# Kernel optimization log

Hardware: AMD Instinct MI355X
Metric: run time of the kernel (lower is better)

The kernel has to match this reference:

```python
import jax, jax.numpy as jnp
import numpy as np
import math

B, N, DIM = 2, 4096, 256
NUM_HEADS = 8
HEAD_DIM = DIM // NUM_HEADS
WINDOW = 7  # default window_size in create_local_mask


def local_mask(seq_len: int, window_size: int = WINDOW) -> jnp.ndarray:
    """Boolean [N,N] mask: True where attention is allowed (2D grid locality)."""
    grid = int(math.isqrt(seq_len))
    idx = jnp.arange(seq_len)
    row, col = idx // grid, idx % grid
    half = window_size // 2
    ok_row = jnp.abs(row[:, None] - row[None, :]) <= half
    ok_col = jnp.abs(col[:, None] - col[None, :]) <= half
    return ok_row & ok_col


def setup_inputs() -> dict:
    key = jax.random.key(0)
    k1, k2, k3, k4 = jax.random.split(key, 4)
    x = jax.random.normal(k1, (B, N, DIM), dtype=jnp.float32)
    W_qkv = jax.random.normal(k2, (3 * DIM, DIM), dtype=jnp.float32) * (DIM ** -0.5)
    W_proj = jax.random.normal(k3, (DIM, DIM), dtype=jnp.float32) * (DIM ** -0.5)
    b_proj = jax.random.normal(k4, (DIM,), dtype=jnp.float32) * 0.01
    temperature = jnp.ones((1,), dtype=jnp.float32)
    return {"x": x, "W_qkv": W_qkv, "W_proj": W_proj, "b_proj": b_proj,
            "temperature": temperature}


def reference(x, W_qkv, W_proj, b_proj, temperature):
    Bb, Nn, C = x.shape
    scale = HEAD_DIM ** -0.5
    # qkv linear (no bias): [B,N,3C] -> [3,B,H,N,hd]
    qkv = (x @ W_qkv.T).reshape(Bb, Nn, 3, NUM_HEADS, HEAD_DIM)
    qkv = jnp.transpose(qkv, (2, 0, 3, 1, 4))
    q, k, v = qkv[0], qkv[1], qkv[2]
    # scores with learnable temperature
    attn = jnp.einsum('bhqd,bhkd->bhqk', q, k) * (scale * temperature[0])
    mask = local_mask(Nn)  # training path: N > 100 -> mask applied
    attn = jnp.where(mask[None, None, :, :], attn, -jnp.inf)
    attn = jax.nn.softmax(attn, axis=-1)
    out = jnp.einsum('bhqk,bhkd->bhqd', attn, v)  # [B,H,N,hd]
    out = jnp.transpose(out, (0, 2, 1, 3)).reshape(Bb, Nn, C)
    return out @ W_proj.T + b_proj
```

## Files before the change

kernel.cpp:

```cpp
#include <hip/hip_runtime.h>
#include <hip/hip_bf16.h>
#include <math.h>

#define DIM   256
#define NHEAD 8
#define HD    32
#define NTOK  4096
#define GRD   64
#define BATCH 2
#define MTOT  (BATCH * NTOK)
#define PLANE (NTOK * HD)

typedef __attribute__((ext_vector_type(8))) short bf16x8;
typedef __attribute__((ext_vector_type(4))) float f32x4;

static __device__ __forceinline__ unsigned short f2b(float f) {
  __hip_bfloat16 h = __float2bfloat16(f);
  union { __hip_bfloat16 h; unsigned short u; } cv;
  cv.h = h;
  return cv.u;
}

static __device__ __forceinline__ unsigned cvtpk_bf16(float lo, float hi) {
  unsigned r;
  asm("v_cvt_pk_bf16_f32 %0, %1, %2" : "=v"(r) : "v"(lo), "v"(hi));
  return r;
}

static __device__ __forceinline__ bf16x8 pack8(float4 a0, float4 a1) {
  union { bf16x8 v; unsigned short u[8]; } o;
  o.u[0] = f2b(a0.x); o.u[1] = f2b(a0.y); o.u[2] = f2b(a0.z); o.u[3] = f2b(a0.w);
  o.u[4] = f2b(a1.x); o.u[5] = f2b(a1.y); o.u[6] = f2b(a1.z); o.u[7] = f2b(a1.w);
  return o.v;
}

#define GLDS16(SRC, DST) __builtin_amdgcn_global_load_lds( \
    (const __attribute__((address_space(1))) void*)(SRC),  \
    (__attribute__((address_space(3))) void*)(DST), 16, 0, 0)

__global__ __launch_bounds__(256) void gemm_qkv(const float* __restrict__ A,
                                                const float* __restrict__ Bw,
                                                unsigned short* __restrict__ Cout) {
  const int K = 256;
  __shared__ __align__(16) char smem[34816];
  __hip_bfloat16* As = (__hip_bfloat16*)smem;
  __hip_bfloat16* Bs = (__hip_bfloat16*)(smem + 10240);
  const int tid = threadIdx.x;
  const int l = tid & 63, w = tid >> 6;
  const int bm = blockIdx.y * 128, bn = blockIdx.x * 128;
  const int wr = w >> 1, wc = w & 1;
  const int lr = l & 15, kh = l >> 4;
  const int lrow = l >> 2, lcol = (l & 3) * 8;

  f32x4 acc[4][4];
  #pragma unroll
  for (int i = 0; i < 4; ++i)
    #pragma unroll
    for (int j = 0; j < 4; ++j)
      acc[i][j] = (f32x4){0.f, 0.f, 0.f, 0.f};

  for (int k0 = 0; k0 < K; k0 += 32) {
    #pragma unroll
    for (int i = 0; i < 2; ++i) {
      const int r0 = (w * 2 + i) * 16;
      const float* ga = A  + (size_t)(bm + r0 + lrow) * K + k0 + lcol;
      const float* gb = Bw + (size_t)(bn + r0 + lrow) * K + k0 + lcol;
      float4 a0 = *(const float4*)ga, a1 = *(const float4*)(ga + 4);
      float4 b0 = *(const float4*)gb, b1 = *(const float4*)(gb + 4);
      *(bf16x8*)&As[(r0 + lrow) * 40 + lcol] = pack8(a0, a1);
      *(bf16x8*)&Bs[(r0 + lrow) * 40 + lcol] = pack8(b0, b1);
    }
    __syncthreads();

    bf16x8 af[4], bfr[4];
    #pragma unroll
    for (int f = 0; f < 4; ++f) {
      af[f]  = *(const bf16x8*)&As[(wr * 64 + f * 16 + lr) * 40 + kh * 8];
      bfr[f] = *(const bf16x8*)&Bs[(wc * 64 + f * 16 + lr) * 40 + kh * 8];
    }
    #pragma unroll
    for (int fi = 0; fi < 4; ++fi)
      #pragma unroll
      for (int fj = 0; fj < 4; ++fj)
        acc[fi][fj] = __builtin_amdgcn_mfma_f32_16x16x32_bf16(af[fi], bfr[fj], acc[fi][fj], 0, 0, 0);
    __syncthreads();
  }

  if (blockIdx.x < 4) {
    #pragma unroll
    for (int fi = 0; fi < 4; ++fi)
      #pragma unroll
      for (int fj = 0; fj < 4; ++fj)
        #pragma unroll
        for (int rr = 0; rr < 4; ++rr) {
          const int m = bm + wr * 64 + fi * 16 + kh * 4 + rr;
          const int n = bn + wc * 64 + fj * 16 + lr;
          const int sel = n >> 8, rem = n & 255;
          const int hh = rem >> 5, d = rem & 31;
          const int bb = m >> 12, tok = m & 4095;
          Cout[(size_t)(sel * 16 + bb * 8 + hh) * PLANE + tok * 32 + d] =
              f2b(acc[fi][fj][rr]);
        }
  } else {
    unsigned short* Ts = (unsigned short*)smem;
    #pragma unroll
    for (int fi = 0; fi < 4; ++fi)
      #pragma unroll
      for (int fj = 0; fj < 4; ++fj)
        #pragma unroll
        for (int rr = 0; rr < 4; ++rr) {
          const int tokl = wr * 64 + fi * 16 + kh * 4 + rr;
          const int dl   = wc * 64 + fj * 16 + lr;
          Ts[tokl * 136 + dl] = f2b(acc[fi][fj][rr]);
        }
    __syncthreads();
    const int dl = tid >> 1, th = (tid & 1) * 64;
    const int dg = (bn - 512) + dl;
    const int hh = dg >> 5, dd = dg & 31;
    const int bb = bm >> 12, tokb = bm & 4095;
    unsigned short* vt = Cout + (size_t)(32 + bb * 8 + hh) * PLANE + dd * 4096 + tokb + th;
    #pragma unroll
    for (int j = 0; j < 8; ++j) {
      union { bf16x8 v; unsigned short u[8]; } o;
      #pragma unroll
      for (int e = 0; e < 8; ++e)
        o.u[e] = Ts[(th + j * 8 + e) * 136 + dl];
      *(bf16x8*)(vt + j * 8) = o.v;
    }
  }
}

__global__ __launch_bounds__(256) void gemm_proj(const __hip_bfloat16* __restrict__ A,
                                                 const float* __restrict__ Bw,
                                                 const float* __restrict__ bias,
                                                 float* __restrict__ Cout) {
  const int K = 256, N = 256;
  __shared__ __hip_bfloat16 As[64 * 32];
  __shared__ __hip_bfloat16 Bs[128 * 40];
  const int tid = threadIdx.x;
  const int l = tid & 63, w = tid >> 6;
  const int bm = blockIdx.y * 64, bn = blockIdx.x * 128;
  const int wr = w >> 1, wc = w & 1;
  const int lr = l & 15, kh = l >> 4;
  const int lrow = tid >> 2, lcol = (tid & 3) * 8;

  f32x4 acc[2][4];
  #pragma unroll
  for (int i = 0; i < 2; ++i)
    #pragma unroll
    for (int j = 0; j < 4; ++j)
      acc[i][j] = (f32x4){0.f, 0.f, 0.f, 0.f};

  for (int k0 = 0; k0 < K; k0 += 32) {
    {
      const __hip_bfloat16* ga = A + (size_t)(bm + lrow) * K + k0 + lcol;
      GLDS16(ga, &As[w * 512]);
    }
    #pragma unroll
    for (int i = 0; i < 2; ++i) {
      const int row = i * 64 + lrow;
      const float* gb = Bw + (size_t)(bn + row) * K + k0 + lcol;
      float4 b0 = *(const float4*)gb, b1 = *(const float4*)(gb + 4);
      *(bf16x8*)&Bs[row * 40 + lcol] = pack8(b0, b1);
    }
    __syncthreads();

    bf16x8 af[2], bfr[4];
    #pragma unroll
    for (int f = 0; f < 2; ++f)
      af[f] = *(const bf16x8*)&As[(wr * 32 + f * 16 + lr) * 32 + kh * 8];
    #pragma unroll
    for (int f = 0; f < 4; ++f)
      bfr[f] = *(const bf16x8*)&Bs[(wc * 64 + f * 16 + lr) * 40 + kh * 8];
    #pragma unroll
    for (int fi = 0; fi < 2; ++fi)
      #pragma unroll
      for (int fj = 0; fj < 4; ++fj)
        acc[fi][fj] = __builtin_amdgcn_mfma_f32_16x16x32_bf16(af[fi], bfr[fj], acc[fi][fj], 0, 0, 0);
    __syncthreads();
  }

  #pragma unroll
  for (int fi = 0; fi < 2; ++fi)
    #pragma unroll
    for (int fj = 0; fj < 4; ++fj)
      #pragma unroll
      for (int rr = 0; rr < 4; ++rr) {
        const int m = bm + wr * 32 + fi * 16 + kh * 4 + rr;
        const int n = bn + wc * 64 + fj * 16 + lr;
        Cout[(size_t)m * N + n] = acc[fi][fj][rr] + bias[n];
      }
}

__global__ __launch_bounds__(512, 4) void local_attn_mfma(
    const unsigned short* __restrict__ qkv, const float* __restrict__ temp,
    unsigned short* __restrict__ attn_out) {
  __shared__ __align__(16) unsigned short Ks[512 * 32];
  __shared__ __align__(16) unsigned short Vt[32 * 512];

  const int P = blockIdx.x;
  const int L = (P & 7) * 64 + (P >> 3);
  const int plane = L >> 5, rp = L & 31;
  const int b = plane >> 3, h = plane & 7;
  const int tid = threadIdx.x;
  const int l = tid & 63, wv = tid >> 6;
  const int qr = wv >> 2, wq = wv & 3;
  const int q15 = l & 15, sg = l >> 4;
  const int r = rp * 2 + qr;

  const float scale = 0.17677669529663687f * temp[0];

  const unsigned short* qplane  = qkv + (size_t)(b * 8 + h) * PLANE;
  const unsigned short* kplane  = qplane + (size_t)16 * PLANE;
  const unsigned short* vtplane = qplane + (size_t)32 * PLANE;

  const int rbase = rp * 2 - 3;

  #pragma unroll
  for (int i = 0; i < 4; ++i) {
    const int ch = i * 512 + tid;
    const int tok = ch >> 2, jjp = ch & 3;
    const int ri = tok >> 6, kloc = tok & 63;
    int row = rbase + ri; row = row < 0 ? 0 : (row > 63 ? 63 : row);
    const int jl = jjp ^ ((tok >> 1) & 3);
    const unsigned short* src = kplane + (size_t)(row * 64 + kloc) * 32 + jl * 8;
    GLDS16(src, &Ks[(i * 512 + (tid & ~63)) * 8]);
  }
  #pragma unroll
  for (int i = 0; i < 4; ++i) {
    const int ch = i * 512 + tid;
    const int d = ch >> 6, chp = ch & 63;
    const int chl = chp ^ (d & 7);
    const int ri = chl >> 3, part = chl & 7;
    int row = rbase + ri; row = row < 0 ? 0 : (row > 63 ? 63 : row);
    const unsigned short* src = vtplane + (size_t)d * 4096 + row * 64 + part * 8;
    GLDS16(src, &Vt[(i * 512 + (tid & ~63)) * 8]);
  }

  const bf16x8 qf = *(const bf16x8*)(qplane + (size_t)(r * 64 + wq * 16 + q15) * 32 + sg * 8);

  __syncthreads();

  const int qcol = wq * 16 + q15;
  float m_run = -INFINITY, l_run = 0.f;
  f32x4 Od[2];
  Od[0] = (f32x4){0.f, 0.f, 0.f, 0.f};
  Od[1] = (f32x4){0.f, 0.f, 0.f, 0.f};
  const f32x4 zf = {0.f, 0.f, 0.f, 0.f};
  const int laA = ((l >> 4) & 1) * 32 + q15;
  const int laB = laA + 16;
  const bool hiG = (l & 32) != 0;

  #pragma unroll
  for (int c = 0; c < 7; ++c) {
    const int rr_c = r - 3 + c;
    if (rr_c >= 0 && rr_c <= 63) {
      const int bri = c + qr;
      f32x4 st[4];
      #pragma unroll
      for (int kt = 0; kt < 4; ++kt) {
        const int tok = bri * 64 + kt * 16 + q15;
        const bf16x8 kf = *(const bf16x8*)((const char*)Ks + tok * 64 +
                                           ((sg ^ ((tok >> 1) & 3)) << 4));
        st[kt] = __builtin_amdgcn_mfma_f32_16x16x32_bf16(kf, qf, zf, 0, 0, 0);
      }
      float mc = -INFINITY;
      #pragma unroll
      for (int kt = 0; kt < 4; ++kt)
        #pragma unroll
        for (int rg = 0; rg < 4; ++rg) {
          const int keyloc = kt * 16 + sg * 4 + rg;
          const bool ok = (unsigned)(keyloc - qcol + 3) <= 6u;
          const float v = ok ? st[kt][rg] * scale : -INFINITY;
          st[kt][rg] = v;
          mc = fmaxf(mc, v);
        }
      mc = fmaxf(mc, __shfl_xor(mc, 16));
      mc = fmaxf(mc, __shfl_xor(mc, 32));
      const float mnew = fmaxf(m_run, mc);
      const float alpha = __expf(m_run - mnew);
      float lc = 0.f;
      #pragma unroll
      for (int kt = 0; kt < 4; ++kt)
        #pragma unroll
        for (int rg = 0; rg < 4; ++rg) {
          const float e = __expf(st[kt][rg] - mnew);
          st[kt][rg] = e;
          lc += e;
        }
      lc += __shfl_xor(lc, 16);
      lc += __shfl_xor(lc, 32);
      l_run = l_run * alpha + lc;
      m_run = mnew;
      Od[0] *= alpha;
      Od[1] *= alpha;

      unsigned pkw[8];
      #pragma unroll
      for (int kt = 0; kt < 4; ++kt) {
        pkw[kt * 2 + 0] = cvtpk_bf16(st[kt][0], st[kt][1]);
        pkw[kt * 2 + 1] = cvtpk_bf16(st[kt][2], st[kt][3]);
      }
      #pragma unroll
      for (int hf = 0; hf < 2; ++hf) {
        unsigned wA[2], wB[2];
        #pragma unroll
        for (int w2 = 0; w2 < 2; ++w2) {
          const unsigned a0 = (unsigned)__shfl((int)pkw[(2 * hf) * 2 + w2], laA);
          const unsigned a1 = (unsigned)__shfl((int)pkw[(2 * hf + 1) * 2 + w2], laA);
          wA[w2] = hiG ? a1 : a0;
          const unsigned b0 = (unsigned)__shfl((int)pkw[(2 * hf) * 2 + w2], laB);
          const unsigned b1 = (unsigned)__shfl((int)pkw[(2 * hf + 1) * 2 + w2], laB);
          wB[w2] = hiG ? b1 : b0;
        }
        union { unsigned u[4]; bf16x8 v; } pf;
        pf.u[0] = wA[0]; pf.u[1] = wA[1]; pf.u[2] = wB[0]; pf.u[3] = wB[1];
        #pragma unroll
        for (int dt = 0; dt < 2; ++dt) {
          const int d = dt * 16 + q15;
          const int chl = bri * 8 + hf * 4 + sg;
          const bf16x8 vf = *(const bf16x8*)((const char*)Vt + d * 1024 +
                                             ((chl ^ (d & 7)) << 4));
          Od[dt] = __builtin_amdgcn_mfma_f32_16x16x32_bf16(vf, pf.v, Od[dt], 0, 0, 0);
        }
      }
    }
  }

  const float invl = 1.0f / l_run;
  #pragma unroll
  for (int dt = 0; dt < 2; ++dt) {
    const unsigned w0 = cvtpk_bf16(Od[dt][0] * invl, Od[dt][1] * invl);
    const unsigned w1 = cvtpk_bf16(Od[dt][2] * invl, Od[dt][3] * invl);
    unsigned short* dst = attn_out + (size_t)(b * 4096 + r * 64 + qcol) * 256 +
                          h * 32 + dt * 16 + sg * 4;
    uint2 uu; uu.x = w0; uu.y = w1;
    *(uint2*)dst = uu;
  }
}

extern "C" void kernel_launch(void* const* d_in, const int* in_sizes, int n_in,
                              void* d_out, int out_size, void* d_ws, size_t ws_size,
                              hipStream_t stream) {
  const float* x     = (const float*)d_in[0];
  const float* Wqkv  = (const float*)d_in[1];
  const float* Wproj = (const float*)d_in[2];
  const float* bproj = (const float*)d_in[3];
  const float* temp  = (const float*)d_in[4];
  float* out = (float*)d_out;

  char* ws = (char*)d_ws;
  unsigned short* qkv_bf  = (unsigned short*)ws;
  __hip_bfloat16* attn_bf = (__hip_bfloat16*)(ws + 25165824);

  {
    dim3 grid(3 * DIM / 128, MTOT / 128);
    gemm_qkv<<<grid, 256, 0, stream>>>(x, Wqkv, qkv_bf);
  }
  local_attn_mfma<<<BATCH * NHEAD * (GRD / 2), 512, 0, stream>>>(
      qkv_bf, temp, (unsigned short*)attn_bf);
  {
    dim3 grid(DIM / 128, MTOT / 64);
    gemm_proj<<<grid, 256, 0, stream>>>(attn_bf, Wproj, bproj, out);
  }
}
```

Before: 45.92 us.

## Widen QKV GEMM K-tile to 64, use exp2 softmax, add MFMA priority hints

```diff
diff --git a/kernel.cpp b/kernel.cpp
--- a/kernel.cpp
+++ b/kernel.cpp
@@ -21,6 +21,10 @@
   return cv.u;
 }
 
+static __device__ __forceinline__ float exp2g(float x) {
+  return __builtin_amdgcn_exp2f(x);
+}
+
 static __device__ __forceinline__ unsigned cvtpk_bf16(float lo, float hi) {
   unsigned r;
   asm("v_cvt_pk_bf16_f32 %0, %1, %2" : "=v"(r) : "v"(lo), "v"(hi));
@@ -42,15 +46,14 @@
                                                 const float* __restrict__ Bw,
                                                 unsigned short* __restrict__ Cout) {
   const int K = 256;
-  __shared__ __align__(16) char smem[34816];
+  __shared__ __align__(16) char smem[73728];
   __hip_bfloat16* As = (__hip_bfloat16*)smem;
-  __hip_bfloat16* Bs = (__hip_bfloat16*)(smem + 10240);
+  __hip_bfloat16* Bs = (__hip_bfloat16*)(smem + 36864);
   const int tid = threadIdx.x;
   const int l = tid & 63, w = tid >> 6;
   const int bm = blockIdx.y * 128, bn = blockIdx.x * 128;
   const int wr = w >> 1, wc = w & 1;
   const int lr = l & 15, kh = l >> 4;
-  const int lrow = l >> 2, lcol = (l & 3) * 8;
 
   f32x4 acc[4][4];
   #pragma unroll
@@ -59,30 +62,34 @@
     for (int j = 0; j < 4; ++j)
       acc[i][j] = (f32x4){0.f, 0.f, 0.f, 0.f};
 
-  for (int k0 = 0; k0 < K; k0 += 32) {
-    #pragma unroll
-    for (int i = 0; i < 2; ++i) {
-      const int r0 = (w * 2 + i) * 16;
-      const float* ga = A  + (size_t)(bm + r0 + lrow) * K + k0 + lcol;
-      const float* gb = Bw + (size_t)(bn + r0 + lrow) * K + k0 + lcol;
+  for (int k0 = 0; k0 < K; k0 += 64) {
+    #pragma unroll
+    for (int i = 0; i < 4; ++i) {
+      const int ch = i * 256 + tid;
+      const int row = ch >> 3, col = (ch & 7) * 8;
+      const float* ga = A  + (size_t)(bm + row) * K + k0 + col;
+      const float* gb = Bw + (size_t)(bn + row) * K + k0 + col;
       float4 a0 = *(const float4*)ga, a1 = *(const float4*)(ga + 4);
       float4 b0 = *(const float4*)gb, b1 = *(const float4*)(gb + 4);
-      *(bf16x8*)&As[(r0 + lrow) * 40 + lcol] = pack8(a0, a1);
-      *(bf16x8*)&Bs[(r0 + lrow) * 40 + lcol] = pack8(b0, b1);
-    }
-    __syncthreads();
-
-    bf16x8 af[4], bfr[4];
-    #pragma unroll
-    for (int f = 0; f < 4; ++f) {
-      af[f]  = *(const bf16x8*)&As[(wr * 64 + f * 16 + lr) * 40 + kh * 8];
-      bfr[f] = *(const bf16x8*)&Bs[(wc * 64 + f * 16 + lr) * 40 + kh * 8];
-    }
-    #pragma unroll
-    for (int fi = 0; fi < 4; ++fi)
-      #pragma unroll
-      for (int fj = 0; fj < 4; ++fj)
-        acc[fi][fj] = __builtin_amdgcn_mfma_f32_16x16x32_bf16(af[fi], bfr[fj], acc[fi][fj], 0, 0, 0);
+      *(bf16x8*)&As[row * 72 + col] = pack8(a0, a1);
+      *(bf16x8*)&Bs[row * 72 + col] = pack8(b0, b1);
+    }
+    __syncthreads();
+
+    #pragma unroll
+    for (int ks = 0; ks < 2; ++ks) {
+      bf16x8 af[4], bfr[4];
+      #pragma unroll
+      for (int f = 0; f < 4; ++f) {
+        af[f]  = *(const bf16x8*)&As[(wr * 64 + f * 16 + lr) * 72 + ks * 32 + kh * 8];
+        bfr[f] = *(const bf16x8*)&Bs[(wc * 64 + f * 16 + lr) * 72 + ks * 32 + kh * 8];
+      }
+      #pragma unroll
+      for (int fi = 0; fi < 4; ++fi)
+        #pragma unroll
+        for (int fj = 0; fj < 4; ++fj)
+          acc[fi][fj] = __builtin_amdgcn_mfma_f32_16x16x32_bf16(af[fi], bfr[fj], acc[fi][fj], 0, 0, 0);
+    }
     __syncthreads();
   }
 
@@ -208,7 +215,7 @@
   const int q15 = l & 15, sg = l >> 4;
   const int r = rp * 2 + qr;
 
-  const float scale = 0.17677669529663687f * temp[0];
+  const float scale2 = 0.17677669529663687f * 1.44269504088896f * temp[0];
 
   const unsigned short* qplane  = qkv + (size_t)(b * 8 + h) * PLANE;
   const unsigned short* kplane  = qplane + (size_t)16 * PLANE;
@@ -257,6 +264,7 @@
     if (rr_c >= 0 && rr_c <= 63) {
       const int bri = c + qr;
       f32x4 st[4];
+      __builtin_amdgcn_s_setprio(1);
       #pragma unroll
       for (int kt = 0; kt < 4; ++kt) {
         const int tok = bri * 64 + kt * 16 + q15;
@@ -264,6 +272,7 @@
                                            ((sg ^ ((tok >> 1) & 3)) << 4));
         st[kt] = __builtin_amdgcn_mfma_f32_16x16x32_bf16(kf, qf, zf, 0, 0, 0);
       }
+      __builtin_amdgcn_s_setprio(0);
       float mc = -INFINITY;
       #pragma unroll
       for (int kt = 0; kt < 4; ++kt)
@@ -271,20 +280,20 @@
         for (int rg = 0; rg < 4; ++rg) {
           const int keyloc = kt * 16 + sg * 4 + rg;
           const bool ok = (unsigned)(keyloc - qcol + 3) <= 6u;
-          const float v = ok ? st[kt][rg] * scale : -INFINITY;
+          const float v = ok ? st[kt][rg] * scale2 : -INFINITY;
           st[kt][rg] = v;
           mc = fmaxf(mc, v);
         }
       mc = fmaxf(mc, __shfl_xor(mc, 16));
       mc = fmaxf(mc, __shfl_xor(mc, 32));
       const float mnew = fmaxf(m_run, mc);
-      const float alpha = __expf(m_run - mnew);
+      const float alpha = exp2g(m_run - mnew);
       float lc = 0.f;
       #pragma unroll
       for (int kt = 0; kt < 4; ++kt)
         #pragma unroll
         for (int rg = 0; rg < 4; ++rg) {
-          const float e = __expf(st[kt][rg] - mnew);
+          const float e = exp2g(st[kt][rg] - mnew);
           st[kt][rg] = e;
           lc += e;
         }
@@ -315,6 +324,7 @@
         }
         union { unsigned u[4]; bf16x8 v; } pf;
         pf.u[0] = wA[0]; pf.u[1] = wA[1]; pf.u[2] = wB[0]; pf.u[3] = wB[1];
+        __builtin_amdgcn_s_setprio(1);
         #pragma unroll
         for (int dt = 0; dt < 2; ++dt) {
           const int d = dt * 16 + q15;
@@ -323,6 +333,7 @@
                                              ((chl ^ (d & 7)) << 4));
           Od[dt] = __builtin_amdgcn_mfma_f32_16x16x32_bf16(vf, pf.v, Od[dt], 0, 0, 0);
         }
+        __builtin_amdgcn_s_setprio(0);
       }
     }
   }
```

New measurement: 45.38 us (median of 3 runs). Within noise of the previous version (-1.2%).
